# Kernel tuning notes

Hardware: AMD Instinct MI355X
Metric: run time of the kernel (lower is better)

The kernel has to match this reference:

```python
import jax, jax.numpy as jnp
import numpy as np

X_WEIGHT = 1.0
Y_WEIGHT = 1.0


def setup_inputs() -> dict:
    key = jax.random.key(0)
    k1, k2 = jax.random.split(key)
    B, C, H, W = 32, 8, 256, 256
    inp = jax.random.normal(k1, (B, C, H, W), dtype=jnp.float32)
    tgt = jax.random.uniform(k2, (B, C, H, W), dtype=jnp.float32)
    return {"input": inp, "target": tgt}


def reference(input, target):
    B, C, H, W = input.shape
    # coordinate maps: x[j] = (j+1 - W/2)/W, y[p] = (p+1 - H/2)/H  (tanh half-range)
    xs = (jnp.arange(W, dtype=jnp.float32) + 1.0 - W / 2.0) / W  # [W]
    ys = (jnp.arange(H, dtype=jnp.float32) + 1.0 - H / 2.0) / H  # [H]

    # DSNT: softmax over each flattened heatmap, then coordinate expectation
    p = jax.nn.softmax(input.reshape(B, C, H * W), axis=-1).reshape(B, C, H, W)
    pred_x = jnp.einsum('bchw,w->bc', p, xs)  # [B, C]
    pred_y = jnp.einsum('bchw,h->bc', p, ys)  # [B, C]

    # ground truth via argmax of target heatmap, converted to same coord range
    idx = jnp.argmax(target.reshape(B, C, H * W), axis=-1)  # [B, C] int
    true_x = ((idx % W).astype(jnp.float32) + 1.0 - W / 2.0) / W
    true_y = ((idx // W).astype(jnp.float32) + 1.0 - H / 2.0) / H

    # per-heatmap MSE over the 2-vector (x, y), each weighted
    dx = pred_x * X_WEIGHT - true_x * X_WEIGHT
    dy = pred_y * Y_WEIGHT - true_y * Y_WEIGHT
    mse = 0.5 * (dx * dx + dy * dy)  # [B, C]

    # original sums over all B*C heatmaps, then divides by B (i+1 == batch size)
    return jnp.sum(mse) / B
```

## Files before the change

### kernel.cpp

```cpp
#include <hip/hip_runtime.h>
#include <math.h>

#define HW 65536
#define NMAPS 256
#define THREADS 1024
#define ITERS (HW / 4 / THREADS)

__device__ __forceinline__ void softmax_merge(float& m, float& s, float& sx, float& sy,
                                              float om, float os, float osx, float osy) {
    const float LOG2E = 1.4426950408889634f;
    float nm = fmaxf(m, om);
    float r1 = __builtin_exp2f((m - nm) * LOG2E);
    float r2 = __builtin_exp2f((om - nm) * LOG2E);
    s  = s * r1 + os * r2;
    sx = sx * r1 + osx * r2;
    sy = sy * r1 + osy * r2;
    m = nm;
}

__global__ __launch_bounds__(THREADS) void dsnt_map_kernel(const float* __restrict__ input,
                                                           const float* __restrict__ target,
                                                           float* __restrict__ ws) {
    const int bc  = blockIdx.x;
    const int tid = threadIdx.x;
    const float4* in4 = (const float4*)(input  + (size_t)bc * HW);
    const float4* tg4 = (const float4*)(target + (size_t)bc * HW);

    const float LOG2E  = 1.4426950408889634f;
    const float INV256 = 1.0f / 256.0f;

    float m = -INFINITY, s = 0.f, sx = 0.f, sy = 0.f;
    float tv = -INFINITY;
    int   ti = 0x7fffffff;

#pragma unroll 4
    for (int it = 0; it < ITERS; ++it) {
        int q = tid + it * THREADS;
        float4 v = in4[q];
        float4 t = tg4[q];

        int h  = q >> 6;
        int w0 = (q & 63) << 2;
        float cy  = (float)(h  - 127) * INV256;
        float cx0 = (float)(w0 - 127) * INV256;

        float m4 = fmaxf(fmaxf(v.x, v.y), fmaxf(v.z, v.w));
        float nm = fmaxf(m, m4);
        float r  = __builtin_exp2f((m - nm) * LOG2E);
        float ns = nm * LOG2E;
        float e0 = __builtin_exp2f(fmaf(v.x, LOG2E, -ns));
        float e1 = __builtin_exp2f(fmaf(v.y, LOG2E, -ns));
        float e2 = __builtin_exp2f(fmaf(v.z, LOG2E, -ns));
        float e3 = __builtin_exp2f(fmaf(v.w, LOG2E, -ns));
        float esum  = (e0 + e1) + (e2 + e3);
        float exsum = fmaf(e0, cx0,
                      fmaf(e1, cx0 + INV256,
                      fmaf(e2, cx0 + 2.f * INV256,
                           e3 * (cx0 + 3.f * INV256))));
        s  = fmaf(s,  r, esum);
        sx = fmaf(sx, r, exsum);
        sy = fmaf(sy, r, esum * cy);
        m = nm;

        int j0 = q << 2;
        if (t.x > tv) { tv = t.x; ti = j0;     }
        if (t.y > tv) { tv = t.y; ti = j0 + 1; }
        if (t.z > tv) { tv = t.z; ti = j0 + 2; }
        if (t.w > tv) { tv = t.w; ti = j0 + 3; }
    }

#pragma unroll
    for (int k = 1; k < 64; k <<= 1) {
        float om  = __shfl_xor(m,  k, 64);
        float os  = __shfl_xor(s,  k, 64);
        float osx = __shfl_xor(sx, k, 64);
        float osy = __shfl_xor(sy, k, 64);
        float otv = __shfl_xor(tv, k, 64);
        int   oti = __shfl_xor(ti, k, 64);
        softmax_merge(m, s, sx, sy, om, os, osx, osy);
        bool take = (otv > tv) || (otv == tv && oti < ti);
        tv = take ? otv : tv;
        ti = take ? oti : ti;
    }

    __shared__ float red_m[16], red_s[16], red_sx[16], red_sy[16], red_tv[16];
    __shared__ int   red_ti[16];
    int wave = tid >> 6, lane = tid & 63;
    if (lane == 0) {
        red_m[wave] = m; red_s[wave] = s; red_sx[wave] = sx; red_sy[wave] = sy;
        red_tv[wave] = tv; red_ti[wave] = ti;
    }
    __syncthreads();
    if (tid == 0) {
        m = red_m[0]; s = red_s[0]; sx = red_sx[0]; sy = red_sy[0];
        tv = red_tv[0]; ti = red_ti[0];
        for (int i = 1; i < 16; ++i) {
            softmax_merge(m, s, sx, sy, red_m[i], red_s[i], red_sx[i], red_sy[i]);
            float otv = red_tv[i]; int oti = red_ti[i];
            if (otv > tv || (otv == tv && oti < ti)) { tv = otv; ti = oti; }
        }
        float px = sx / s, py = sy / s;
        float tx = (float)((ti & 255) - 127) * INV256;
        float ty = (float)((ti >> 8)  - 127) * INV256;
        float dx = px - tx, dy = py - ty;
        ws[bc] = 0.5f * (dx * dx + dy * dy);
    }
}

__global__ __launch_bounds__(NMAPS) void dsnt_final_reduce(const float* __restrict__ ws,
                                                           float* __restrict__ out) {
    int tid = threadIdx.x;
    float v = ws[tid];
#pragma unroll
    for (int k = 32; k > 0; k >>= 1) v += __shfl_down(v, k, 64);
    __shared__ float partial[4];
    int wave = tid >> 6, lane = tid & 63;
    if (lane == 0) partial[wave] = v;
    __syncthreads();
    if (tid == 0) {
        float total = (partial[0] + partial[1]) + (partial[2] + partial[3]);
        out[0] = total * (1.0f / 32.0f);
    }
}

extern "C" void kernel_launch(void* const* d_in, const int* in_sizes, int n_in,
                              void* d_out, int out_size, void* d_ws, size_t ws_size,
                              hipStream_t stream) {
    const float* input  = (const float*)d_in[0];
    const float* target = (const float*)d_in[1];
    float* ws  = (float*)d_ws;
    float* out = (float*)d_out;

    dsnt_map_kernel<<<NMAPS, THREADS, 0, stream>>>(input, target, ws);
    dsnt_final_reduce<<<1, NMAPS, 0, stream>>>(ws, out);
}
```

Measured before the change: 145.8 us.

## Split each heatmap into chunks and separate softmax and argmax into distinct blocks

The work is repartitioned from one 1024-thread block per heatmap (256 blocks) into 4096 small 256-thread blocks. Each block handles one eighth of a map and does either the online-softmax coordinate sums or the target argmax, and loads all of its float4s up front. The partial softmax and argmax states go to workspace and are merged by the final single-block kernel, which also computes the loss. This is meant to fill all CUs with more in-flight memory requests than 256 blocks can, at the cost of more workspace traffic and a heavier final merge.

```diff
diff --git a/kernel.cpp b/kernel.cpp
--- a/kernel.cpp
+++ b/kernel.cpp
@@ -3,8 +3,10 @@
 
 #define HW 65536
 #define NMAPS 256
-#define THREADS 1024
-#define ITERS (HW / 4 / THREADS)
+#define THREADS 256
+#define CHUNKS 8
+#define F4_PER_CHUNK 2048
+#define F4_PER_THREAD 8
 
 __device__ __forceinline__ void softmax_merge(float& m, float& s, float& sx, float& sy,
                                               float om, float os, float osx, float osy) {
@@ -18,106 +20,144 @@
     m = nm;
 }
 
-__global__ __launch_bounds__(THREADS) void dsnt_map_kernel(const float* __restrict__ input,
-                                                           const float* __restrict__ target,
-                                                           float* __restrict__ ws) {
-    const int bc  = blockIdx.x;
-    const int tid = threadIdx.x;
-    const float4* in4 = (const float4*)(input  + (size_t)bc * HW);
-    const float4* tg4 = (const float4*)(target + (size_t)bc * HW);
+__global__ __launch_bounds__(THREADS, 8) void dsnt_pass1(const float* __restrict__ input,
+                                                         const float* __restrict__ target,
+                                                         float4* __restrict__ wsA,
+                                                         float2* __restrict__ wsB) {
+    const int b    = blockIdx.x;
+    const int role = b & 1;
+    const int id   = b >> 1;
+    const int map  = id >> 3;
+    const int chunk = id & 7;
+    const int tid  = threadIdx.x;
+    const int wave = tid >> 6, lane = tid & 63;
 
     const float LOG2E  = 1.4426950408889634f;
+    const float INV256 = 1.0f / 256.0f;
+
+    __shared__ float red0[4], red1[4], red2[4], red3[4];
+    __shared__ int   red4[4];
+
+    if (role == 0) {
+        const float4* p = (const float4*)(input + (size_t)map * HW) + chunk * F4_PER_CHUNK;
+        float4 v[F4_PER_THREAD];
+#pragma unroll
+        for (int k = 0; k < F4_PER_THREAD; ++k) v[k] = p[tid + k * THREADS];
+
+        float m = -INFINITY, s = 0.f, sx = 0.f, sy = 0.f;
+#pragma unroll
+        for (int k = 0; k < F4_PER_THREAD; ++k) {
+            int Q  = chunk * F4_PER_CHUNK + tid + k * THREADS;
+            int h  = Q >> 6;
+            int w0 = (Q & 63) << 2;
+            float cy  = (float)(h  - 127) * INV256;
+            float cx0 = (float)(w0 - 127) * INV256;
+            float4 vv = v[k];
+
+            float m4 = fmaxf(fmaxf(vv.x, vv.y), fmaxf(vv.z, vv.w));
+            float nm = fmaxf(m, m4);
+            float r  = __builtin_exp2f((m - nm) * LOG2E);
+            float ns = nm * LOG2E;
+            float e0 = __builtin_exp2f(fmaf(vv.x, LOG2E, -ns));
+            float e1 = __builtin_exp2f(fmaf(vv.y, LOG2E, -ns));
+            float e2 = __builtin_exp2f(fmaf(vv.z, LOG2E, -ns));
+            float e3 = __builtin_exp2f(fmaf(vv.w, LOG2E, -ns));
+            float esum  = (e0 + e1) + (e2 + e3);
+            float exsum = fmaf(e0, cx0,
+                          fmaf(e1, cx0 + INV256,
+                          fmaf(e2, cx0 + 2.f * INV256,
+                               e3 * (cx0 + 3.f * INV256))));
+            s  = fmaf(s,  r, esum);
+            sx = fmaf(sx, r, exsum);
+            sy = fmaf(sy, r, esum * cy);
+            m  = nm;
+        }
+
+#pragma unroll
+        for (int k = 1; k < 64; k <<= 1) {
+            float om  = __shfl_xor(m,  k, 64);
+            float os  = __shfl_xor(s,  k, 64);
+            float osx = __shfl_xor(sx, k, 64);
+            float osy = __shfl_xor(sy, k, 64);
+            softmax_merge(m, s, sx, sy, om, os, osx, osy);
+        }
+        if (lane == 0) { red0[wave] = m; red1[wave] = s; red2[wave] = sx; red3[wave] = sy; }
+        __syncthreads();
+        if (tid == 0) {
+            m = red0[0]; s = red1[0]; sx = red2[0]; sy = red3[0];
+            for (int i = 1; i < 4; ++i)
+                softmax_merge(m, s, sx, sy, red0[i], red1[i], red2[i], red3[i]);
+            wsA[id] = make_float4(m, s, sx, sy);
+        }
+    } else {
+        const float4* p = (const float4*)(target + (size_t)map * HW) + chunk * F4_PER_CHUNK;
+        float4 t[F4_PER_THREAD];
+#pragma unroll
+        for (int k = 0; k < F4_PER_THREAD; ++k) t[k] = p[tid + k * THREADS];
+
+        float tv = -INFINITY;
+        int   ti = 0x7fffffff;
+#pragma unroll
+        for (int k = 0; k < F4_PER_THREAD; ++k) {
+            int Q  = chunk * F4_PER_CHUNK + tid + k * THREADS;
+            int j0 = Q << 2;
+            float4 tt = t[k];
+            if (tt.x > tv) { tv = tt.x; ti = j0;     }
+            if (tt.y > tv) { tv = tt.y; ti = j0 + 1; }
+            if (tt.z > tv) { tv = tt.z; ti = j0 + 2; }
+            if (tt.w > tv) { tv = tt.w; ti = j0 + 3; }
+        }
+#pragma unroll
+        for (int k = 1; k < 64; k <<= 1) {
+            float otv = __shfl_xor(tv, k, 64);
+            int   oti = __shfl_xor(ti, k, 64);
+            bool take = (otv > tv) || (otv == tv && oti < ti);
+            tv = take ? otv : tv;
+            ti = take ? oti : ti;
+        }
+        if (lane == 0) { red0[wave] = tv; red4[wave] = ti; }
+        __syncthreads();
+        if (tid == 0) {
+            tv = red0[0]; ti = red4[0];
+            for (int i = 1; i < 4; ++i) {
+                float otv = red0[i]; int oti = red4[i];
+                if (otv > tv || (otv == tv && oti < ti)) { tv = otv; ti = oti; }
+            }
+            wsB[id] = make_float2(tv, __int_as_float(ti));
+        }
+    }
+}
+
+__global__ __launch_bounds__(NMAPS) void dsnt_pass2(const float4* __restrict__ wsA,
+                                                    const float2* __restrict__ wsB,
+                                                    float* __restrict__ out) {
+    const int t = threadIdx.x;
     const float INV256 = 1.0f / 256.0f;
 
     float m = -INFINITY, s = 0.f, sx = 0.f, sy = 0.f;
     float tv = -INFINITY;
     int   ti = 0x7fffffff;
-
-#pragma unroll 4
-    for (int it = 0; it < ITERS; ++it) {
-        int q = tid + it * THREADS;
-        float4 v = in4[q];
-        float4 t = tg4[q];
-
-        int h  = q >> 6;
-        int w0 = (q & 63) << 2;
-        float cy  = (float)(h  - 127) * INV256;
-        float cx0 = (float)(w0 - 127) * INV256;
-
-        float m4 = fmaxf(fmaxf(v.x, v.y), fmaxf(v.z, v.w));
-        float nm = fmaxf(m, m4);
-        float r  = __builtin_exp2f((m - nm) * LOG2E);
-        float ns = nm * LOG2E;
-        float e0 = __builtin_exp2f(fmaf(v.x, LOG2E, -ns));
-        float e1 = __builtin_exp2f(fmaf(v.y, LOG2E, -ns));
-        float e2 = __builtin_exp2f(fmaf(v.z, LOG2E, -ns));
-        float e3 = __builtin_exp2f(fmaf(v.w, LOG2E, -ns));
-        float esum  = (e0 + e1) + (e2 + e3);
-        float exsum = fmaf(e0, cx0,
-                      fmaf(e1, cx0 + INV256,
-                      fmaf(e2, cx0 + 2.f * INV256,
-                           e3 * (cx0 + 3.f * INV256))));
-        s  = fmaf(s,  r, esum);
-        sx = fmaf(sx, r, exsum);
-        sy = fmaf(sy, r, esum * cy);
-        m = nm;
-
-        int j0 = q << 2;
-        if (t.x > tv) { tv = t.x; ti = j0;     }
-        if (t.y > tv) { tv = t.y; ti = j0 + 1; }
-        if (t.z > tv) { tv = t.z; ti = j0 + 2; }
-        if (t.w > tv) { tv = t.w; ti = j0 + 3; }
+#pragma unroll
+    for (int c = 0; c < CHUNKS; ++c) {
+        float4 a = wsA[t * CHUNKS + c];
+        softmax_merge(m, s, sx, sy, a.x, a.y, a.z, a.w);
+        float2 bb = wsB[t * CHUNKS + c];
+        int oti = __float_as_int(bb.y);
+        if (bb.x > tv || (bb.x == tv && oti < ti)) { tv = bb.x; ti = oti; }
     }
+    float px = sx / s, py = sy / s;
+    float tx = (float)((ti & 255) - 127) * INV256;
+    float ty = (float)((ti >> 8)  - 127) * INV256;
+    float dx = px - tx, dy = py - ty;
+    float loss = 0.5f * (dx * dx + dy * dy);
 
 #pragma unroll
-    for (int k = 1; k < 64; k <<= 1) {
-        float om  = __shfl_xor(m,  k, 64);
-        float os  = __shfl_xor(s,  k, 64);
-        float osx = __shfl_xor(sx, k, 64);
-        float osy = __shfl_xor(sy, k, 64);
-        float otv = __shfl_xor(tv, k, 64);
-        int   oti = __shfl_xor(ti, k, 64);
-        softmax_merge(m, s, sx, sy, om, os, osx, osy);
-        bool take = (otv > tv) || (otv == tv && oti < ti);
-        tv = take ? otv : tv;
-        ti = take ? oti : ti;
-    }
-
-    __shared__ float red_m[16], red_s[16], red_sx[16], red_sy[16], red_tv[16];
-    __shared__ int   red_ti[16];
-    int wave = tid >> 6, lane = tid & 63;
-    if (lane == 0) {
-        red_m[wave] = m; red_s[wave] = s; red_sx[wave] = sx; red_sy[wave] = sy;
-        red_tv[wave] = tv; red_ti[wave] = ti;
-    }
+    for (int k = 32; k > 0; k >>= 1) loss += __shfl_down(loss, k, 64);
+    __shared__ float partial[4];
+    int wave = t >> 6, lane = t & 63;
+    if (lane == 0) partial[wave] = loss;
     __syncthreads();
-    if (tid == 0) {
-        m = red_m[0]; s = red_s[0]; sx = red_sx[0]; sy = red_sy[0];
-        tv = red_tv[0]; ti = red_ti[0];
-        for (int i = 1; i < 16; ++i) {
-            softmax_merge(m, s, sx, sy, red_m[i], red_s[i], red_sx[i], red_sy[i]);
-            float otv = red_tv[i]; int oti = red_ti[i];
-            if (otv > tv || (otv == tv && oti < ti)) { tv = otv; ti = oti; }
-        }
-        float px = sx / s, py = sy / s;
-        float tx = (float)((ti & 255) - 127) * INV256;
-        float ty = (float)((ti >> 8)  - 127) * INV256;
-        float dx = px - tx, dy = py - ty;
-        ws[bc] = 0.5f * (dx * dx + dy * dy);
-    }
-}
-
-__global__ __launch_bounds__(NMAPS) void dsnt_final_reduce(const float* __restrict__ ws,
-                                                           float* __restrict__ out) {
-    int tid = threadIdx.x;
-    float v = ws[tid];
-#pragma unroll
-    for (int k = 32; k > 0; k >>= 1) v += __shfl_down(v, k, 64);
-    __shared__ float partial[4];
-    int wave = tid >> 6, lane = tid & 63;
-    if (lane == 0) partial[wave] = v;
-    __syncthreads();
-    if (tid == 0) {
+    if (t == 0) {
         float total = (partial[0] + partial[1]) + (partial[2] + partial[3]);
         out[0] = total * (1.0f / 32.0f);
     }
@@ -128,9 +168,10 @@
                               hipStream_t stream) {
     const float* input  = (const float*)d_in[0];
     const float* target = (const float*)d_in[1];
-    float* ws  = (float*)d_ws;
-    float* out = (float*)d_out;
+    float4* wsA = (float4*)d_ws;
+    float2* wsB = (float2*)((char*)d_ws + 2048 * sizeof(float4));
+    float*  out = (float*)d_out;
 
-    dsnt_map_kernel<<<NMAPS, THREADS, 0, stream>>>(input, target, ws);
-    dsnt_final_reduce<<<1, NMAPS, 0, stream>>>(ws, out);
+    dsnt_pass1<<<2 * 2048, THREADS, 0, stream>>>(input, target, wsA, wsB);
+    dsnt_pass2<<<1, NMAPS, 0, stream>>>(wsA, wsB, out);
 }
```

Result: no change. 144.1 us (-1.2%).
